# Optimization experiments

Hardware: AMD Instinct MI355X
Metric: run time of the kernel (lower is better)

## Reference

```python
import jax, jax.numpy as jnp
import numpy as np

MAX_REL = 64  # max_relative_position
LN_EPS = 1e-5


def _relative_positions(seq_len):
    r = jnp.arange(seq_len)
    rel = jnp.clip(r[None, :] - r[:, None], -MAX_REL, MAX_REL) + MAX_REL
    return rel  # [S, S] int32 in [0, 2*MAX_REL]


def setup_inputs() -> dict:
    key = jax.random.key(0)
    ks = jax.random.split(key, 8)
    B, S, H = 8, 1024, 128
    sd = 1.0 / np.sqrt(H)
    return {
        "x": jax.random.normal(ks[0], (B, S, H), jnp.float32),
        "Wq": jax.random.normal(ks[1], (H, H), jnp.float32) * sd,
        "bq": jnp.zeros((H,), jnp.float32),
        "Wk": jax.random.normal(ks[2], (H, H), jnp.float32) * sd,
        "bk": jnp.zeros((H,), jnp.float32),
        "Wv": jax.random.normal(ks[3], (H, H), jnp.float32) * sd,
        "bv": jnp.zeros((H,), jnp.float32),
        "rel_k": jax.random.normal(ks[4], (2 * MAX_REL + 1, H), jnp.float32),
        "rel_v": jax.random.normal(ks[5], (2 * MAX_REL + 1, H), jnp.float32),
        "Wo": jax.random.normal(ks[6], (H, H), jnp.float32) * sd,
        "bo": jnp.zeros((H,), jnp.float32),
        "gamma": jnp.ones((H,), jnp.float32),
        "beta": jnpp if False else jnp.zeros((H,), jnp.float32),
    }


def reference(x, Wq, bq, Wk, bk, Wv, bv, rel_k, rel_v, Wo, bo, gamma, beta):
    B, S, H = x.shape
    scale = jnp.sqrt(jnp.asarray(H, x.dtype))

    q = x @ Wq + bq  # [B,S,H]
    k = x @ Wk + bk
    v = x @ Wv + bv

    scores = jnp.einsum("bih,bjh->bij", q, k) / scale  # [B,S,S]

    relpos = _relative_positions(S)            # [S,S] int
    rk = rel_k[relpos]                          # [S,S,H] gather
    scores = scores + jnp.einsum("bih,ijh->bij", q, rk)

    attn = jax.nn.softmax(scores, axis=-1)      # dropout = identity (eval)

    ctx = jnp.einsum("bij,bjh->bih", attn, v)
    rv = rel_v[relpos]                          # [S,S,H] gather
    ctx = ctx + jnp.einsum("bij,ijh->bih", attn, rv)

    out = ctx @ Wo + bo

    # residual + LayerNorm
    y = out + x
    mu = jnp.mean(y, axis=-1, keepdims=True)
    var = jnp.mean(jnp.square(y - mu), axis=-1, keepdims=True)
    y = (y - mu) * jax.lax.rsqrt(var + LN_EPS) * gamma + beta
    return y, attn
```

## Files before the change

### kernel.cpp

```cpp
#include <hip/hip_runtime.h>

constexpr int Bn = 8, Sn = 1024, Hn = 128, Rn = 129;
constexpr float INV_SCALE = 0.088388347648318447f;
constexpr size_t YEL = (size_t)Bn * Sn * Hn;

typedef short bf16x8 __attribute__((ext_vector_type(8)));
typedef short v4s __attribute__((ext_vector_type(4)));
typedef float f32x4 __attribute__((ext_vector_type(4)));
typedef int v4i __attribute__((ext_vector_type(4)));

__device__ __forceinline__ float bf2f(short s) {
    unsigned u = ((unsigned)(unsigned short)s) << 16;
    float f; __builtin_memcpy(&f, &u, 4); return f;
}
__device__ __forceinline__ short f2bf(float f) {
    unsigned u; __builtin_memcpy(&u, &f, 4);
    unsigned r = (u + 0x7fffu + ((u >> 16) & 1u)) >> 16;
    return (short)(r & 0xffffu);
}

__device__ __forceinline__ void gll16(const short* g, short* l) {
    __builtin_amdgcn_global_load_lds(
        (const __attribute__((address_space(1))) void*)g,
        (__attribute__((address_space(3))) void*)l, 16, 0, 0);
}

__global__ __launch_bounds__(384) void build_tables(
    const float* __restrict__ rel_k, const float* __restrict__ rel_v,
    const float* __restrict__ Wo,
    const float* __restrict__ Wq, const float* __restrict__ Wk,
    const float* __restrict__ Wv,
    short* __restrict__ relcat, short* __restrict__ BcatT,
    short* __restrict__ wtab)
{
    if (blockIdx.x < Rn) {
        const int p = blockIdx.x, c = threadIdx.x;
        const int j = (c < 256) ? (c & 127) : (c - 256);
        float v = rel_k[p * Hn + j];
        short h = f2bf(v);
        relcat[p * 384 + c] = (c < 256) ? h : f2bf(v - bf2f(h));
    } else if (blockIdx.x < Rn + 107) {
        int idx = (blockIdx.x - Rn) * 384 + threadIdx.x;
        if (idx < 320 * 128) {
            int k = idx >> 7, n = idx & 127;
            float v;
            if (k < 128) v = Wo[k * Hn + n];
            else if (k < 257) {
                int p = k - 128; float a = 0.f;
                for (int h = 0; h < Hn; ++h) a += rel_v[p * Hn + h] * Wo[h * Hn + n];
                v = a;
            } else v = 0.f;
            BcatT[n * 320 + k] = f2bf(v);
        }
    } else {
        int idx = (blockIdx.x - Rn - 107) * 384 + threadIdx.x;
        int sel = idx >> 14, rem = idx & 16383;
        int n = rem >> 7, k = rem & 127;
        const float* W = (sel == 0) ? Wq : (sel == 1) ? Wk : Wv;
        float v = W[k * Hn + n];
        short h = f2bf(v);
        wtab[sel * 32768 + n * 128 + k] = h;
        wtab[sel * 32768 + 16384 + n * 128 + k] = f2bf(v - bf2f(h));
    }
}

__global__ __launch_bounds__(256) void proj(
    const float* __restrict__ X, const short* __restrict__ wtab,
    const float* __restrict__ bq, const float* __restrict__ bk,
    const float* __restrict__ bv,
    short* __restrict__ qcat, short* __restrict__ kh, short* __restrict__ vT)
{
    __shared__ float xs[64][128];
    const int tid = threadIdx.x;
    const int sel = blockIdx.y;
    const int row0 = blockIdx.x * 64;
    const float* bias = (sel == 0) ? bq : (sel == 1) ? bk : bv;
    const short* wh = wtab + sel * 32768;
    const short* wl = wh + 16384;

#pragma unroll
    for (int it = 0; it < 8; ++it) {
        int u = tid + it * 256;
        int r = u >> 5, c4 = (u & 31) * 4;
        *(float4*)&xs[r][c4] = *(const float4*)(X + (size_t)(row0 + r) * 128 + c4);
    }
    __syncthreads();

    const int w = tid >> 6, lane = tid & 63;
    const int quad = lane >> 4, l15 = lane & 15;

    bf16x8 xh[4], xl[4];
#pragma unroll
    for (int kk = 0; kk < 4; ++kk) {
#pragma unroll
        for (int j = 0; j < 8; ++j) {
            float v = xs[w * 16 + l15][kk * 32 + quad * 8 + j];
            short h = f2bf(v);
            xh[kk][j] = h;
            xl[kk][j] = f2bf(v - bf2f(h));
        }
    }

    f32x4 acc[8] = {};
#pragma unroll
    for (int nt = 0; nt < 8; ++nt) {
        const short* bh = wh + (size_t)(nt * 16 + l15) * 128;
        const short* bl = wl + (size_t)(nt * 16 + l15) * 128;
#pragma unroll
        for (int kk = 0; kk < 4; ++kk) {
            bf16x8 bhf = *(const bf16x8*)(bh + kk * 32 + quad * 8);
            bf16x8 blf = *(const bf16x8*)(bl + kk * 32 + quad * 8);
            acc[nt] = __builtin_amdgcn_mfma_f32_16x16x32_bf16(xh[kk], bhf, acc[nt], 0, 0, 0);
            acc[nt] = __builtin_amdgcn_mfma_f32_16x16x32_bf16(xh[kk], blf, acc[nt], 0, 0, 0);
            acc[nt] = __builtin_amdgcn_mfma_f32_16x16x32_bf16(xl[kk], bhf, acc[nt], 0, 0, 0);
        }
    }

#pragma unroll
    for (int nt = 0; nt < 8; ++nt) {
        int col = nt * 16 + l15;
        float bv2 = bias[col];
#pragma unroll
        for (int r = 0; r < 4; ++r) {
            int row = row0 + w * 16 + quad * 4 + r;
            float v = acc[nt][r] + bv2;
            short h = f2bf(v);
            if (sel == 0) {
                qcat[(size_t)row * 256 + col] = h;
                qcat[(size_t)row * 256 + 128 + col] = f2bf(v - bf2f(h));
            } else if (sel == 1) {
                kh[(size_t)row * 128 + col] = h;
            } else {
                int b = row >> 10, i = row & (Sn - 1);
                vT[(size_t)b * 131072 + (size_t)col * 1024 + i] = h;
            }
        }
    }
}

__global__ __launch_bounds__(512, 4) void fused_attn(
    const short* __restrict__ qcat, const short* __restrict__ kh,
    const short* __restrict__ vT, const short* __restrict__ relcat,
    const short* __restrict__ BcatT,
    const float* __restrict__ X, const float* __restrict__ bo,
    const float* __restrict__ gamma, const float* __restrict__ beta,
    float* __restrict__ attn_g, float* __restrict__ y_g)
{
    __shared__ __align__(16) char smem[78848];
    short* bufS = (short*)smem;
    short* Pb   = (short*)(smem + 32768);
    short* CtxA = (short*)(smem + 65792);
    float* QrL  = (float*)(smem + 65792);
    float* redM = (float*)(smem + 76800);
    float* redS = redM + 128;
    float* redL = redS + 128;
    float* redH = redL + 128;

    const int tid = threadIdx.x;
    const int w = tid >> 6, lane = tid & 63;
    const int quad = lane >> 4, l15 = lane & 15;
    const int lb = blockIdx.x + (blockIdx.z << 6);
    const int bz = lb & 7;
    const int row0 = (lb >> 3) << 4;
    const size_t grow0 = (size_t)bz * Sn + row0;

    const short* khb  = kh + (size_t)bz * Sn * 128;
    const short* vtb0 = vT + (size_t)bz * 131072;

    auto stage_kh = [&](int kt2) {
        const short* base = khb + (size_t)((kt2 >> 1) * 128) * 128 + (kt2 & 1) * 64;
        short* dst = bufS + (kt2 & 1) * 8192;
#pragma unroll
        for (int it = 0; it < 2; ++it) {
            int g = tid + it * 512;
            int r = g >> 3, c = g & 7;
            gll16(base + r * 128 + ((c ^ (r & 7)) * 8), dst + g * 8);
        }
    };
    auto stage_v = [&](int kc2) {
        const short* base = vtb0 + (kc2 >> 1) * 128 + (kc2 & 1) * 64;
        short* dst = bufS + (kc2 & 1) * 8192;
#pragma unroll
        for (int it = 0; it < 2; ++it) {
            int g = tid + it * 512;
            int r = g >> 3, c = g & 7;
            gll16(base + r * 1024 + ((c ^ (r & 7)) * 8), dst + g * 8);
        }
    };

    stage_kh(0);

    bf16x8 afr[4];
#pragma unroll
    for (int kk = 0; kk < 4; ++kk)
        afr[kk] = *(const bf16x8*)(qcat + (grow0 + l15) * 256 + kk * 32 + quad * 8);

    {
        const short* aq = qcat + (grow0 + l15) * 256;
        const short* br = relcat + (size_t)(w * 16 + l15) * 384;
        const short* br2 = relcat + (size_t)(128 + l15) * 384;
        f32x4 qacc = {};
        f32x4 qacc2 = {};
#pragma unroll
        for (int ks = 0; ks < 12; ++ks) {
            int koff = ks * 32 + quad * 8;
            int srcc = (koff >= 256) ? koff - 256 : koff;
            bf16x8 qa = *(const bf16x8*)(aq + srcc);
            bf16x8 qb = *(const bf16x8*)(br + ks * 32 + quad * 8);
            qacc = __builtin_amdgcn_mfma_f32_16x16x32_bf16(qa, qb, qacc, 0, 0, 0);
            if (w == 0) {
                bf16x8 qb2 = *(const bf16x8*)(br2 + ks * 32 + quad * 8);
                qacc2 = __builtin_amdgcn_mfma_f32_16x16x32_bf16(qa, qb2, qacc2, 0, 0, 0);
            }
        }
#pragma unroll
        for (int r = 0; r < 4; ++r)
            QrL[(quad * 4 + r) * 132 + w * 16 + l15] = qacc[r];
        if (w == 0 && l15 == 0) {
#pragma unroll
            for (int r = 0; r < 4; ++r)
                QrL[(quad * 4 + r) * 132 + 128] = qacc2[r];
        }
    }
    __syncthreads();

    f32x4 acc[8] = {};
#pragma unroll
    for (int kt2 = 0; kt2 < 16; ++kt2) {
        if (kt2 < 15) stage_kh(kt2 + 1);
        const short* hb = bufS + (kt2 & 1) * 8192;
        const int rb = w * 16 + l15;
#pragma unroll
        for (int kk = 0; kk < 2; ++kk) {
            int j = (kk * 4 + quad) ^ (l15 & 7);
            bf16x8 b = *(const bf16x8*)(hb + rb * 64 + j * 8);
            acc[kt2 >> 1] = __builtin_amdgcn_mfma_f32_16x16x32_bf16(
                afr[(kt2 & 1) * 2 + kk], b, acc[kt2 >> 1], 0, 0, 0);
        }
        __syncthreads();
    }

    stage_v(0);

    float mx[4];
#pragma unroll
    for (int r = 0; r < 4; ++r) {
        int lr = quad * 4 + r, i = row0 + lr;
        float m = -3.4e38f;
#pragma unroll
        for (int kt = 0; kt < 8; ++kt) {
            int col = kt * 128 + w * 16 + l15;
            int d = col - i; d = (d < -64) ? -64 : (d > 64 ? 64 : d);
            float v = acc[kt][r] * INV_SCALE + QrL[lr * 132 + d + 64];
            acc[kt][r] = v;
            m = fmaxf(m, v);
        }
#pragma unroll
        for (int msk = 1; msk < 16; msk <<= 1) m = fmaxf(m, __shfl_xor(m, msk));
        if (l15 == 0) redM[lr * 8 + w] = m;
    }
    __syncthreads();
#pragma unroll
    for (int r = 0; r < 4; ++r) {
        int lr = quad * 4 + r;
        float m = redM[lr * 8];
#pragma unroll
        for (int j = 1; j < 8; ++j) m = fmaxf(m, redM[lr * 8 + j]);
        mx[r] = m;
    }

#pragma unroll
    for (int r = 0; r < 4; ++r) {
        int lr = quad * 4 + r, i = row0 + lr;
        float s = 0.f, lo = 0.f, hi = 0.f;
#pragma unroll
        for (int kt = 0; kt < 8; ++kt) {
            float e = __expf(acc[kt][r] - mx[r]);
            acc[kt][r] = e;
            s += e;
            int col = kt * 128 + w * 16 + l15;
            lo += (col <= i - 64) ? e : 0.f;
            hi += (col >= i + 64) ? e : 0.f;
        }
#pragma unroll
        for (int msk = 1; msk < 16; msk <<= 1) {
            s += __shfl_xor(s, msk);
            lo += __shfl_xor(lo, msk);
            hi += __shfl_xor(hi, msk);
        }
        if (l15 == 0) { redS[lr * 8 + w] = s; redL[lr * 8 + w] = lo; redH[lr * 8 + w] = hi; }
    }
    __syncthreads();

#pragma unroll
    for (int r = 0; r < 4; ++r) {
        int lr = quad * 4 + r;
        float s = 0.f;
#pragma unroll
        for (int j = 0; j < 8; ++j) s += redS[lr * 8 + j];
        float inv = 1.0f / s;
#pragma unroll
        for (int kt = 0; kt < 8; ++kt) {
            int col = kt * 128 + w * 16 + l15;
            Pb[lr * 1032 + col] = f2bf(acc[kt][r] * inv);
        }
    }
    __syncthreads();

    {
        float* ab = attn_g + grow0 * Sn;
#pragma unroll
        for (int it = 0; it < 8; ++it) {
            int u = tid + it * 512;
            int r = u >> 8, c4 = (u & 255) * 4;
            v4s pv = *(const v4s*)&Pb[r * 1032 + c4];
            f32x4 o;
            o[0] = bf2f(pv[0]); o[1] = bf2f(pv[1]);
            o[2] = bf2f(pv[2]); o[3] = bf2f(pv[3]);
            __builtin_nontemporal_store(o, (f32x4*)(ab + (size_t)r * Sn + c4));
        }
    }

    f32x4 cacc = {};
#pragma unroll
    for (int kc2 = 0; kc2 < 16; ++kc2) {
        if (kc2 < 15) stage_v(kc2 + 1);
        const short* hb = bufS + (kc2 & 1) * 8192;
        const int rb = w * 16 + l15;
#pragma unroll
        for (int kk = 0; kk < 2; ++kk) {
            bf16x8 a = *(const bf16x8*)&Pb[l15 * 1032 + kc2 * 64 + kk * 32 + quad * 8];
            int j = (kk * 4 + quad) ^ (l15 & 7);
            bf16x8 b = *(const bf16x8*)(hb + rb * 64 + j * 8);
            cacc = __builtin_amdgcn_mfma_f32_16x16x32_bf16(a, b, cacc, 0, 0, 0);
        }
        __syncthreads();
    }

#pragma unroll
    for (int r = 0; r < 4; ++r)
        CtxA[(quad * 4 + r) * 344 + w * 16 + l15] = f2bf(cacc[r]);
#pragma unroll
    for (int rr = 0; rr < 2; ++rr) {
        int lr = w * 2 + rr, i = row0 + lr;
        float s = 0.f, lo = 0.f, hi = 0.f;
#pragma unroll
        for (int j = 0; j < 8; ++j) {
            s += redS[lr * 8 + j]; lo += redL[lr * 8 + j]; hi += redH[lr * 8 + j];
        }
        float inv = 1.0f / s;
        float v0;
        if (lane == 0) v0 = lo * inv;
        else { int c = i + lane - 64; v0 = (c >= 0 && c < Sn) ? bf2f(Pb[lr * 1032 + c]) : 0.f; }
        CtxA[lr * 344 + 128 + lane] = f2bf(v0);
        int c1 = i + lane;
        CtxA[lr * 344 + 192 + lane] = (c1 < Sn) ? Pb[lr * 1032 + c1] : (short)0;
        CtxA[lr * 344 + 256 + lane] = (lane == 0) ? f2bf(hi * inv) : (short)0;
    }
    __syncthreads();

    f32x4 yacc = {};
    const short* bcb = BcatT + (size_t)(w * 16 + l15) * 320;
#pragma unroll
    for (int ch = 0; ch < 3; ++ch) {
        const int nkk = (ch == 2) ? 2 : 4;
#pragma unroll
        for (int kk = 0; kk < 4; ++kk) {
            if (kk >= nkk) break;
            bf16x8 a = *(const bf16x8*)&CtxA[l15 * 344 + ch * 128 + kk * 32 + quad * 8];
            bf16x8 b = *(const bf16x8*)(bcb + ch * 128 + kk * 32 + quad * 8);
            yacc = __builtin_amdgcn_mfma_f32_16x16x32_bf16(a, b, yacc, 0, 0, 0);
        }
    }

    const int col = w * 16 + l15;
    const float bov = bo[col], gv = gamma[col], bev = beta[col];
    float vv[4];
#pragma unroll
    for (int r = 0; r < 4; ++r) {
        int lr = quad * 4 + r;
        vv[r] = yacc[r] + bov + X[(grow0 + lr) * 128 + col];
    }
#pragma unroll
    for (int r = 0; r < 4; ++r) {
        float s = vv[r];
#pragma unroll
        for (int msk = 1; msk < 16; msk <<= 1) s += __shfl_xor(s, msk);
        if (l15 == 0) redM[(quad * 4 + r) * 8 + w] = s;
    }
    __syncthreads();
    float mu[4];
#pragma unroll
    for (int r = 0; r < 4; ++r) {
        int lr = quad * 4 + r;
        float s = 0.f;
#pragma unroll
        for (int j = 0; j < 8; ++j) s += redM[lr * 8 + j];
        mu[r] = s * (1.f / 128.f);
    }
#pragma unroll
    for (int r = 0; r < 4; ++r) {
        float d = vv[r] - mu[r];
        float s = d * d;
#pragma unroll
        for (int msk = 1; msk < 16; msk <<= 1) s += __shfl_xor(s, msk);
        if (l15 == 0) redS[(quad * 4 + r) * 8 + w] = s;
    }
    __syncthreads();
#pragma unroll
    for (int r = 0; r < 4; ++r) {
        int lr = quad * 4 + r;
        float s = 0.f;
#pragma unroll
        for (int j = 0; j < 8; ++j) s += redS[lr * 8 + j];
        float inv = rsqrtf(s * (1.f / 128.f) + 1e-5f);
        float yv = (vv[r] - mu[r]) * inv * gv + bev;
        __builtin_nontemporal_store(yv, &y_g[(grow0 + lr) * 128 + col]);
    }
}

extern "C" void kernel_launch(void* const* d_in, const int* in_sizes, int n_in,
                              void* d_out, int out_size, void* d_ws, size_t ws_size,
                              hipStream_t stream) {
    const float* x     = (const float*)d_in[0];
    const float* Wq    = (const float*)d_in[1];
    const float* bq    = (const float*)d_in[2];
    const float* Wk    = (const float*)d_in[3];
    const float* bk    = (const float*)d_in[4];
    const float* Wv    = (const float*)d_in[5];
    const float* bv    = (const float*)d_in[6];
    const float* rel_k = (const float*)d_in[7];
    const float* rel_v = (const float*)d_in[8];
    const float* Wo    = (const float*)d_in[9];
    const float* bo    = (const float*)d_in[10];
    const float* gamma = (const float*)d_in[11];
    const float* beta  = (const float*)d_in[12];

    char* ws = (char*)d_ws;
    short* kh     = (short*)(ws + 0);
    short* vT     = (short*)(ws + 2097152);
    short* qcat   = (short*)(ws + 4194304);
    short* relcat = (short*)(ws + 8388608);
    short* BcatT  = (short*)(ws + 8519680);
    short* wtab   = (short*)(ws + 8650752);

    float* y_out = (float*)d_out;
    float* attn  = (float*)d_out + YEL;

    build_tables<<<dim3(Rn + 107 + 128), 384, 0, stream>>>(
        rel_k, rel_v, Wo, Wq, Wk, Wv, relcat, BcatT, wtab);
    proj<<<dim3(128, 3), 256, 0, stream>>>(x, wtab, bq, bk, bv, qcat, kh, vT);

    fused_attn<<<dim3(64, 1, Bn), 512, 0, stream>>>(
        qcat, kh, vT, relcat, BcatT, x, bo, gamma, beta, attn, y_out);
}
```

Baseline: 154.7 us.

## Deepen K/V staging to 4-stage ring with vmcnt waits and defer attn store

Replaces the double-buffered 64-wide K and V staging with a four-slot ring of 32-wide chunks. Each step issues one global-to-LDS load per thread and waits with explicit vmcnt counts and a raw s_barrier, so two loads stay in flight instead of a full sync after every tile. The fp32 attention-probability store is moved after the PV, output projection and LayerNorm stages, so its global writes no longer sit in front of the V loop. The price is more barriers (32 per loop instead of 16), a new swizzle pattern, and reliance on hand-tuned waitcnt correctness.

```diff
diff --git a/kernel.cpp b/kernel.cpp
--- a/kernel.cpp
+++ b/kernel.cpp
@@ -167,28 +167,21 @@
     const short* khb  = kh + (size_t)bz * Sn * 128;
     const short* vtb0 = vT + (size_t)bz * 131072;
 
-    auto stage_kh = [&](int kt2) {
-        const short* base = khb + (size_t)((kt2 >> 1) * 128) * 128 + (kt2 & 1) * 64;
-        short* dst = bufS + (kt2 & 1) * 8192;
-#pragma unroll
-        for (int it = 0; it < 2; ++it) {
-            int g = tid + it * 512;
-            int r = g >> 3, c = g & 7;
-            gll16(base + r * 128 + ((c ^ (r & 7)) * 8), dst + g * 8);
-        }
+    auto stage_khq = [&](int j) {
+        int t = j >> 2, q = j & 3;
+        int rr = tid >> 2, c = tid & 3;
+        gll16(khb + (size_t)(t * 128 + rr) * 128 + q * 32 + ((c ^ ((rr >> 1) & 3)) * 8),
+              bufS + (j & 3) * 4096 + tid * 8);
     };
-    auto stage_v = [&](int kc2) {
-        const short* base = vtb0 + (kc2 >> 1) * 128 + (kc2 & 1) * 64;
-        short* dst = bufS + (kc2 & 1) * 8192;
-#pragma unroll
-        for (int it = 0; it < 2; ++it) {
-            int g = tid + it * 512;
-            int r = g >> 3, c = g & 7;
-            gll16(base + r * 1024 + ((c ^ (r & 7)) * 8), dst + g * 8);
-        }
+    auto stage_vq = [&](int j) {
+        int t = j >> 2, q = j & 3;
+        int rr = tid >> 2, c = tid & 3;
+        gll16(vtb0 + (size_t)rr * 1024 + t * 128 + q * 32 + ((c ^ ((rr >> 1) & 3)) * 8),
+              bufS + (j & 3) * 4096 + tid * 8);
     };
 
-    stage_kh(0);
+    stage_khq(0);
+    stage_khq(1);
 
     bf16x8 afr[4];
 #pragma unroll
@@ -224,23 +217,31 @@
     }
     __syncthreads();
 
+    const int rb = w * 16 + l15;
+    const int jsw = quad ^ ((l15 >> 1) & 3);
     f32x4 acc[8] = {};
 #pragma unroll
-    for (int kt2 = 0; kt2 < 16; ++kt2) {
-        if (kt2 < 15) stage_kh(kt2 + 1);
-        const short* hb = bufS + (kt2 & 1) * 8192;
-        const int rb = w * 16 + l15;
-#pragma unroll
-        for (int kk = 0; kk < 2; ++kk) {
-            int j = (kk * 4 + quad) ^ (l15 & 7);
-            bf16x8 b = *(const bf16x8*)(hb + rb * 64 + j * 8);
-            acc[kt2 >> 1] = __builtin_amdgcn_mfma_f32_16x16x32_bf16(
-                afr[(kt2 & 1) * 2 + kk], b, acc[kt2 >> 1], 0, 0, 0);
-        }
-        __syncthreads();
-    }
-
-    stage_v(0);
+    for (int r = 0; r < 32; ++r) {
+        if (r < 30) {
+            stage_khq(r + 2);
+            __builtin_amdgcn_sched_barrier(0);
+            asm volatile("s_waitcnt vmcnt(2)" ::: "memory");
+        } else if (r == 30) {
+            asm volatile("s_waitcnt vmcnt(1)" ::: "memory");
+        } else {
+            asm volatile("s_waitcnt vmcnt(0)" ::: "memory");
+        }
+        __builtin_amdgcn_sched_barrier(0);
+        __builtin_amdgcn_s_barrier();
+        __builtin_amdgcn_sched_barrier(0);
+        const short* hb = bufS + (r & 3) * 4096;
+        bf16x8 b = *(const bf16x8*)(hb + rb * 32 + jsw * 8);
+        acc[r >> 2] = __builtin_amdgcn_mfma_f32_16x16x32_bf16(
+            afr[r & 3], b, acc[r >> 2], 0, 0, 0);
+    }
+
+    stage_vq(0);
+    stage_vq(1);
 
     float mx[4];
 #pragma unroll
@@ -306,6 +307,108 @@
         }
     }
     __syncthreads();
+
+    f32x4 cacc = {};
+#pragma unroll
+    for (int r = 0; r < 32; ++r) {
+        if (r < 30) {
+            stage_vq(r + 2);
+            __builtin_amdgcn_sched_barrier(0);
+            asm volatile("s_waitcnt vmcnt(2)" ::: "memory");
+        } else if (r == 30) {
+            asm volatile("s_waitcnt vmcnt(1)" ::: "memory");
+        } else {
+            asm volatile("s_waitcnt vmcnt(0)" ::: "memory");
+        }
+        __builtin_amdgcn_sched_barrier(0);
+        __builtin_amdgcn_s_barrier();
+        __builtin_amdgcn_sched_barrier(0);
+        const short* hb = bufS + (r & 3) * 4096;
+        bf16x8 a = *(const bf16x8*)&Pb[l15 * 1032 + r * 32 + quad * 8];
+        bf16x8 b = *(const bf16x8*)(hb + rb * 32 + jsw * 8);
+        cacc = __builtin_amdgcn_mfma_f32_16x16x32_bf16(a, b, cacc, 0, 0, 0);
+    }
+
+#pragma unroll
+    for (int r = 0; r < 4; ++r)
+        CtxA[(quad * 4 + r) * 344 + w * 16 + l15] = f2bf(cacc[r]);
+#pragma unroll
+    for (int rr = 0; rr < 2; ++rr) {
+        int lr = w * 2 + rr, i = row0 + lr;
+        float s = 0.f, lo = 0.f, hi = 0.f;
+#pragma unroll
+        for (int j = 0; j < 8; ++j) {
+            s += redS[lr * 8 + j]; lo += redL[lr * 8 + j]; hi += redH[lr * 8 + j];
+        }
+        float inv = 1.0f / s;
+        float v0;
+        if (lane == 0) v0 = lo * inv;
+        else { int c = i + lane - 64; v0 = (c >= 0 && c < Sn) ? bf2f(Pb[lr * 1032 + c]) : 0.f; }
+        CtxA[lr * 344 + 128 + lane] = f2bf(v0);
+        int c1 = i + lane;
+        CtxA[lr * 344 + 192 + lane] = (c1 < Sn) ? Pb[lr * 1032 + c1] : (short)0;
+        CtxA[lr * 344 + 256 + lane] = (lane == 0) ? f2bf(hi * inv) : (short)0;
+    }
+    __syncthreads();
+
+    f32x4 yacc = {};
+    const short* bcb = BcatT + (size_t)(w * 16 + l15) * 320;
+#pragma unroll
+    for (int ch = 0; ch < 3; ++ch) {
+        const int nkk = (ch == 2) ? 2 : 4;
+#pragma unroll
+        for (int kk = 0; kk < 4; ++kk) {
+            if (kk >= nkk) break;
+            bf16x8 a = *(const bf16x8*)&CtxA[l15 * 344 + ch * 128 + kk * 32 + quad * 8];
+            bf16x8 b = *(const bf16x8*)(bcb + ch * 128 + kk * 32 + quad * 8);
+            yacc = __builtin_amdgcn_mfma_f32_16x16x32_bf16(a, b, yacc, 0, 0, 0);
+        }
+    }
+
+    const int col = w * 16 + l15;
+    const float bov = bo[col], gv = gamma[col], bev = beta[col];
+    float vv[4];
+#pragma unroll
+    for (int r = 0; r < 4; ++r) {
+        int lr = quad * 4 + r;
+        vv[r] = yacc[r] + bov + X[(grow0 + lr) * 128 + col];
+    }
+#pragma unroll
+    for (int r = 0; r < 4; ++r) {
+        float s = vv[r];
+#pragma unroll
+        for (int msk = 1; msk < 16; msk <<= 1) s += __shfl_xor(s, msk);
+        if (l15 == 0) redM[(quad * 4 + r) * 8 + w] = s;
+    }
+    __syncthreads();
+    float mu[4];
+#pragma unroll
+    for (int r = 0; r < 4; ++r) {
+        int lr = quad * 4 + r;
+        float s = 0.f;
+#pragma unroll
+        for (int j = 0; j < 8; ++j) s += redM[lr * 8 + j];
+        mu[r] = s * (1.f / 128.f);
+    }
+#pragma unroll
+    for (int r = 0; r < 4; ++r) {
+        float d = vv[r] - mu[r];
+        float s = d * d;
+#pragma unroll
+        for (int msk = 1; msk < 16; msk <<= 1) s += __shfl_xor(s, msk);
+        if (l15 == 0) redS[(quad * 4 + r) * 8 + w] = s;
+    }
+    __syncthreads();
+#pragma unroll
+    for (int r = 0; r < 4; ++r) {
+        int lr = quad * 4 + r;
+        float s = 0.f;
+#pragma unroll
+        for (int j = 0; j < 8; ++j) s += redS[lr * 8 + j];
+        float inv = rsqrtf(s * (1.f / 128.f) + 1e-5f);
+        float yv = (vv[r] - mu[r]) * inv * gv + bev;
+        __builtin_nontemporal_store(yv, &y_g[(grow0 + lr) * 128 + col]);
+    }
 
     {
         float* ab = attn_g + grow0 * Sn;
@@ -319,103 +422,6 @@
             o[2] = bf2f(pv[2]); o[3] = bf2f(pv[3]);
             __builtin_nontemporal_store(o, (f32x4*)(ab + (size_t)r * Sn + c4));
         }
-    }
-
-    f32x4 cacc = {};
-#pragma unroll
-    for (int kc2 = 0; kc2 < 16; ++kc2) {
-        if (kc2 < 15) stage_v(kc2 + 1);
-        const short* hb = bufS + (kc2 & 1) * 8192;
-        const int rb = w * 16 + l15;
-#pragma unroll
-        for (int kk = 0; kk < 2; ++kk) {
-            bf16x8 a = *(const bf16x8*)&Pb[l15 * 1032 + kc2 * 64 + kk * 32 + quad * 8];
-            int j = (kk * 4 + quad) ^ (l15 & 7);
-            bf16x8 b = *(const bf16x8*)(hb + rb * 64 + j * 8);
-            cacc = __builtin_amdgcn_mfma_f32_16x16x32_bf16(a, b, cacc, 0, 0, 0);
-        }
-        __syncthreads();
-    }
-
-#pragma unroll
-    for (int r = 0; r < 4; ++r)
-        CtxA[(quad * 4 + r) * 344 + w * 16 + l15] = f2bf(cacc[r]);
-#pragma unroll
-    for (int rr = 0; rr < 2; ++rr) {
-        int lr = w * 2 + rr, i = row0 + lr;
-        float s = 0.f, lo = 0.f, hi = 0.f;
-#pragma unroll
-        for (int j = 0; j < 8; ++j) {
-            s += redS[lr * 8 + j]; lo += redL[lr * 8 + j]; hi += redH[lr * 8 + j];
-        }
-        float inv = 1.0f / s;
-        float v0;
-        if (lane == 0) v0 = lo * inv;
-        else { int c = i + lane - 64; v0 = (c >= 0 && c < Sn) ? bf2f(Pb[lr * 1032 + c]) : 0.f; }
-        CtxA[lr * 344 + 128 + lane] = f2bf(v0);
-        int c1 = i + lane;
-        CtxA[lr * 344 + 192 + lane] = (c1 < Sn) ? Pb[lr * 1032 + c1] : (short)0;
-        CtxA[lr * 344 + 256 + lane] = (lane == 0) ? f2bf(hi * inv) : (short)0;
-    }
-    __syncthreads();
-
-    f32x4 yacc = {};
-    const short* bcb = BcatT + (size_t)(w * 16 + l15) * 320;
-#pragma unroll
-    for (int ch = 0; ch < 3; ++ch) {
-        const int nkk = (ch == 2) ? 2 : 4;
-#pragma unroll
-        for (int kk = 0; kk < 4; ++kk) {
-            if (kk >= nkk) break;
-            bf16x8 a = *(const bf16x8*)&CtxA[l15 * 344 + ch * 128 + kk * 32 + quad * 8];
-            bf16x8 b = *(const bf16x8*)(bcb + ch * 128 + kk * 32 + quad * 8);
-            yacc = __builtin_amdgcn_mfma_f32_16x16x32_bf16(a, b, yacc, 0, 0, 0);
-        }
-    }
-
-    const int col = w * 16 + l15;
-    const float bov = bo[col], gv = gamma[col], bev = beta[col];
-    float vv[4];
-#pragma unroll
-    for (int r = 0; r < 4; ++r) {
-        int lr = quad * 4 + r;
-        vv[r] = yacc[r] + bov + X[(grow0 + lr) * 128 + col];
-    }
-#pragma unroll
-    for (int r = 0; r < 4; ++r) {
-        float s = vv[r];
-#pragma unroll
-        for (int msk = 1; msk < 16; msk <<= 1) s += __shfl_xor(s, msk);
-        if (l15 == 0) redM[(quad * 4 + r) * 8 + w] = s;
-    }
-    __syncthreads();
-    float mu[4];
-#pragma unroll
-    for (int r = 0; r < 4; ++r) {
-        int lr = quad * 4 + r;
-        float s = 0.f;
-#pragma unroll
-        for (int j = 0; j < 8; ++j) s += redM[lr * 8 + j];
-        mu[r] = s * (1.f / 128.f);
-    }
-#pragma unroll
-    for (int r = 0; r < 4; ++r) {
-        float d = vv[r] - mu[r];
-        float s = d * d;
-#pragma unroll
-        for (int msk = 1; msk < 16; msk <<= 1) s += __shfl_xor(s, msk);
-        if (l15 == 0) redS[(quad * 4 + r) * 8 + w] = s;
-    }
-    __syncthreads();
-#pragma unroll
-    for (int r = 0; r < 4; ++r) {
-        int lr = quad * 4 + r;
-        float s = 0.f;
-#pragma unroll
-        for (int j = 0; j < 8; ++j) s += redS[lr * 8 + j];
-        float inv = rsqrtf(s * (1.f / 128.f) + 1e-5f);
-        float yv = (vv[r] - mu[r]) * inv * gv + bev;
-        __builtin_nontemporal_store(yv, &y_g[(grow0 + lr) * 128 + col]);
     }
 }
 
```

New measurement: 156.5 us. Within noise of the previous version (+1.2%).
